# Kernel optimization log

Hardware: AMD Instinct MI355X
Metric: run time of the kernel (lower is better)

## Reference

```python
import jax, jax.numpy as jnp
import numpy as np

WS = 8       # window size
NH = 6       # num heads
SHIFT = 4    # ws//2 since index=1 (shifted)
EPS = 1e-6


def _rel_pos_index(ws):
    coords = np.stack(np.meshgrid(np.arange(ws), np.arange(ws), indexing='ij'))  # (2,ws,ws)
    cf = coords.reshape(2, -1)
    rel = (cf[:, :, None] - cf[:, None, :]).transpose(1, 2, 0)  # (N,N,2)
    rel[..., 0] += ws - 1
    rel[..., 1] += ws - 1
    rel[..., 0] *= 2 * ws - 1
    return rel.sum(-1)  # (N,N) int


def _attn_mask(H, W, ws, shift):
    img = np.zeros((H, W))
    slices = (slice(0, -ws), slice(-ws, -shift), slice(-shift, None))
    cnt = 0
    for h in slices:
        for w in slices:
            img[h, w] = cnt
            cnt += 1
    mw = img.reshape(H // ws, ws, W // ws, ws).transpose(0, 2, 1, 3).reshape(-1, ws * ws)
    am = mw[:, None, :] - mw[:, :, None]  # (nW,N,N): unsqueeze(1) - unsqueeze(2)
    return np.where(am != 0, -100.0, 0.0).astype(np.float32)


def layernorm2d(x, w, b):
    mu = x.mean(1, keepdims=True)
    var = ((x - mu) ** 2).mean(1, keepdims=True)
    y = (x - mu) / jnp.sqrt(var + EPS)
    return w[None, :, None, None] * y + b[None, :, None, None]


def window_partition(x, ws):
    B, C, H, W = x.shape
    x = x.reshape(B, C, H // ws, ws, W // ws, ws)
    return x.transpose(0, 2, 4, 3, 5, 1).reshape(-1, ws * ws, C)


def window_reverse(win, ws, H, W):
    B = win.shape[0] // ((H // ws) * (W // ws))
    x = win.reshape(B, H // ws, W // ws, ws, ws, -1)
    return x.transpose(0, 5, 1, 3, 2, 4).reshape(B, -1, H, W)


def shifted_window_attn(x, qkv_w, qkv_b, proj_w, proj_b, rpb_table):
    B, C, H, W = x.shape
    N = WS * WS
    hd = C // NH
    scale = hd ** -0.5
    # faithful to original: raw reshape BCHW->BHWC (reinterpretation), roll, reshape back
    x = jnp.roll(x.reshape(B, H, W, C), (-SHIFT, -SHIFT), (1, 2)).reshape(B, C, H, W)
    win = window_partition(x, WS)  # (B_, N, C)
    B_ = win.shape[0]
    qkv = (win @ qkv_w + qkv_b).reshape(B_, N, 3, NH, hd).transpose(2, 0, 3, 1, 4)
    q, k, v = qkv[0] * scale, qkv[1], qkv[2]
    attn = jnp.einsum('bhnd,bhmd->bhnm', q, k)  # (B_,NH,N,N)
    rpi = _rel_pos_index(WS)
    bias = rpb_table[rpi.reshape(-1)].reshape(N, N, NH).transpose(2, 0, 1)
    attn = attn + bias[None]
    mask = jnp.asarray(_attn_mask(H, W, WS, SHIFT))  # (nW,N,N)
    nW = mask.shape[0]
    attn = attn.reshape(B_ // nW, nW, NH, N, N) + mask[None, :, None]
    attn = jax.nn.softmax(attn.reshape(B_, NH, N, N), axis=-1)
    out = jnp.einsum('bhnm,bhmd->bhnd', attn, v).transpose(0, 2, 1, 3).reshape(B_, N, C)
    out = out @ proj_w + proj_b
    return window_reverse(out, WS, H, W)


def channel_attention(y, ca_w, ca_b):
    gap = y.mean((2, 3))  # (B,C)
    s = jnp.einsum('bc,oc->bo', gap, ca_w) + ca_b  # 1x1 conv on pooled feature
    return s[:, :, None, None]


def mlp(y, fc1_w, fc1_b, fc2_w, fc2_b):
    B, C, H, W = y.shape
    t = y.transpose(0, 2, 3, 1)  # (B,H,W,C)
    t = jax.nn.gelu(t @ fc1_w + fc1_b, approximate=False)
    t = t @ fc2_w + fc2_b
    return t.transpose(0, 3, 1, 2)


def setup_inputs() -> dict:
    key = jax.random.key(0)
    ks = jax.random.split(key, 8)
    C, H, W, B = 192, 256, 256, 2
    hid = 2 * C
    sc = 0.02
    return {
        'x': jax.random.normal(ks[0], (B, C, H, W), jnp.float32),
        'norm1_w': jnp.ones((C,), jnp.float32),
        'norm1_b': jnp.zeros((C,), jnp.float32),
        'qkv_w': jax.random.normal(ks[1], (C, 3 * C), jnp.float32) * sc,
        'qkv_b': jnp.zeros((3 * C,), jnp.float32),
        'proj_w': jax.random.normal(ks[2], (C, C), jnp.float32) * sc,
        'proj_b': jnp.zeros((C,), jnp.float32),
        'rpb_table': jax.random.normal(ks[3], ((2 * WS - 1) ** 2, NH), jnp.float32) * sc,
        'ca_w': jax.random.normal(ks[4], (C, C), jnp.float32) * sc,
        'ca_b': jnp.zeros((C,), jnp.float32),
        'norm2_w': jnp.ones((C,), jnp.float32),
        'norm2_b': jnp.zeros((C,), jnp.float32),
        'fc1_w': jax.random.normal(ks[5], (C, hid), jnp.float32) * sc,
        'fc1_b': jnp.zeros((hid,), jnp.float32),
        'fc2_w': jax.random.normal(ks[6], (hid, C), jnp.float32) * sc,
        'fc2_b': jnp.zeros((C,), jnp.float32),
    }


def reference(x, norm1_w, norm1_b, qkv_w, qkv_b, proj_w, proj_b, rpb_table,
              ca_w, ca_b, norm2_w, norm2_b, fc1_w, fc1_b, fc2_w, fc2_b):
    y = layernorm2d(x, norm1_w, norm1_b)
    y = shifted_window_attn(y, qkv_w, qkv_b, proj_w, proj_b, rpb_table)
    y = y * channel_attention(y, ca_w, ca_b)
    x = x + y
    y2 = mlp(layernorm2d(x, norm2_w, norm2_b), fc1_w, fc1_b, fc2_w, fc2_b)
    return x + y2
```

## Files before the change

kernel.cpp:

```cpp
#include <hip/hip_runtime.h>
#include <hip/hip_bf16.h>
#include <stdint.h>

#define C_   192
#define H_   256
#define W_   256
#define HW_  65536
#define CHW  12582912
#define NH_  6
#define HID_ 384

typedef __attribute__((ext_vector_type(8))) __bf16 bf16x8;
typedef __attribute__((ext_vector_type(8))) uint16_t u16x8;
typedef __attribute__((ext_vector_type(4))) float  fx4;

__device__ __forceinline__ uint16_t f2bf(float f) {
  uint32_t u = __builtin_bit_cast(uint32_t, f);
  u += 0x7fffu + ((u >> 16) & 1u);
  return (uint16_t)(u >> 16);
}
__device__ __forceinline__ float bf2f(uint16_t h) {
  uint32_t u = ((uint32_t)h) << 16;
  return __builtin_bit_cast(float, u);
}
__device__ __forceinline__ uint32_t pk2(float a, float b) {
  return (uint32_t)f2bf(a) | ((uint32_t)f2bf(b) << 16);
}
__device__ __forceinline__ bf16x8 ld8(const uint16_t* p) {
  uint4 v = *reinterpret_cast<const uint4*>(p);
  return __builtin_bit_cast(bf16x8, v);
}
__device__ __forceinline__ fx4 mfma16(bf16x8 a, bf16x8 b, fx4 c) {
  return __builtin_amdgcn_mfma_f32_16x16x32_bf16(a, b, c, 0, 0, 0);
}
__device__ __forceinline__ float gelu_f(float v) {
  float c2 = v * v;
  float u = __builtin_fmaf(c2, 0.044715f, 1.0f) * v;
  float e = exp2f(u * 2.3022084f);
  float th = 1.0f - 2.0f * __builtin_amdgcn_rcpf(1.0f + e);
  float hv = 0.5f * v;
  return __builtin_fmaf(hv, th, hv);
}

__global__ __launch_bounds__(256) void prep_kernel(
    const float* __restrict__ qkv_w, const float* __restrict__ proj_w,
    const float* __restrict__ fc1_w, const float* __restrict__ fc2_w,
    const float* __restrict__ rpb, const float* __restrict__ n2w,
    const float* __restrict__ n2b, const float* __restrict__ fc1_b,
    uint16_t* __restrict__ qkv_wt, uint16_t* __restrict__ proj_wt,
    uint16_t* __restrict__ fc1_wt, uint16_t* __restrict__ fc2_wt,
    float* __restrict__ rpbb, float* __restrict__ b1f) {
  int tid = blockIdx.x * 256 + threadIdx.x;
  if (tid < 576 * 192) {
    int f = tid / 192, k = tid % 192;
    qkv_wt[tid] = f2bf(qkv_w[k * 576 + f]);
  }
  int t1 = tid - 576 * 192;
  if (t1 >= 0 && t1 < 192 * 192) {
    int f = t1 / 192, k = t1 % 192;
    proj_wt[t1] = f2bf(proj_w[k * 192 + f]);
  }
  int t2 = t1 - 192 * 192;
  if (t2 >= 0 && t2 < 384 * 192) {
    int f = t2 / 192, k = t2 % 192;
    fc1_wt[t2] = f2bf(fc1_w[k * 384 + f] * n2w[k]);
  }
  int t3 = t2 - 384 * 192;
  if (t3 >= 0 && t3 < 192 * 384) {
    int f = t3 / 384, k = t3 % 384;
    fc2_wt[t3] = f2bf(fc2_w[k * 192 + f]);
  }
  int t4 = t3 - 192 * 384;
  if (t4 >= 0 && t4 < 6 * 64 * 64) {
    int h = t4 / 4096, nm = t4 % 4096, n = nm / 64, m = nm % 64;
    int yn = n >> 3, xn = n & 7, ym = m >> 3, xm = m & 7;
    int idx = (yn - ym + 7) * 15 + (xn - xm + 7);
    rpbb[t4] = rpb[idx * NH_ + h];
  }
  int t5 = t4 - 6 * 64 * 64;
  if (t5 >= 0 && t5 < 384) {
    float acc = fc1_b[t5];
    for (int c = 0; c < 192; c++) acc = __builtin_fmaf(n2b[c], fc1_w[c * 384 + t5], acc);
    b1f[t5] = acc;
  }
}

__global__ __launch_bounds__(256) void ln1_stats(const float* __restrict__ x,
                                                 float* __restrict__ mu,
                                                 float* __restrict__ rsig) {
  int t = blockIdx.x * 256 + threadIdx.x;
  int b = t >> 16, hw = t & 65535;
  const float* xp = x + (size_t)b * CHW + hw;
  float s = 0.f, sq = 0.f;
#pragma unroll 8
  for (int c = 0; c < C_; c++) {
    float v = xp[(size_t)c * HW_];
    s += v; sq += v * v;
  }
  float m = s * (1.0f / C_);
  float var = sq * (1.0f / C_) - m * m;
  mu[t] = m;
  rsig[t] = rsqrtf(var + 1e-6f);
}

__global__ __launch_bounds__(256) void ln1_apply_kernel(
    const float* __restrict__ x, const float* __restrict__ mu, const float* __restrict__ rsig,
    const float* __restrict__ n1w, const float* __restrict__ n1b,
    uint16_t* __restrict__ y_tok) {
  __shared__ __attribute__((aligned(16))) uint16_t tile[192 * 66];
  int wg = blockIdx.x;
  int b = wg >> 10, hw0 = (wg & 1023) << 6;
  int t = threadIdx.x;
  const float* xb = x + (size_t)b * CHW;
  const float* mub = mu + b * HW_;
  const float* rsb = rsig + b * HW_;
#pragma unroll 4
  for (int it = 0; it < 48; it++) {
    int id = it * 256 + t;
    int ca = id >> 6, pp = id & 63;
    int g = ca * 65536 + hw0 + pp;
    int h2 = g / 49152;
    int r = g - h2 * 49152;
    int w2 = r / 192;
    int c2 = r - w2 * 192;
    int f = ((h2 + 4) & 255) * 49152 + ((w2 + 4) & 255) * 192 + c2;
    int cnat = f >> 16;
    int hwn = f & 65535;
    float v = (xb[f] - mub[hwn]) * rsb[hwn] * n1w[cnat] + n1b[cnat];
    tile[ca * 66 + pp] = f2bf(v);
  }
  __syncthreads();
  uint16_t* yb = y_tok + ((size_t)(b * HW_ + hw0)) * C_;
#pragma unroll 4
  for (int it = 0; it < 48; it++) {
    int id = it * 256 + t;
    int pp = id / 192, ca = id - pp * 192;
    yb[id] = tile[ca * 66 + pp];
  }
}

__global__ __launch_bounds__(256, 2) void attn_kernel(
    const uint16_t* __restrict__ y_tok, const uint16_t* __restrict__ qkv_wt,
    const float* __restrict__ qkv_b, const uint16_t* __restrict__ proj_wt,
    const float* __restrict__ proj_b, const float* __restrict__ rpbb,
    uint16_t* __restrict__ y_attn, float* __restrict__ part) {
  __shared__ __attribute__((aligned(16))) uint16_t Qs[64 * 200];
  __shared__ __attribute__((aligned(16))) uint16_t Ks[64 * 200];
  __shared__ __attribute__((aligned(16))) uint16_t VT[32 * 72];
  __shared__ __attribute__((aligned(16))) uint16_t Ps[64 * 72];
  const int wg = blockIdx.x;
  const int b = wg >> 10, wid = wg & 1023;
  const int wh = wid >> 5, ww = wid & 31;
  const int t = threadIdx.x;
  const int w = t >> 6, l = t & 63;
  const int lane16 = l & 15, quad = l >> 4;
  const int trow = w * 16 + quad * 4;

  bf16x8 afr[4][6];
#pragma unroll
  for (int m = 0; m < 4; m++) {
    const int tok = m * 16 + lane16;
    const uint16_t* ap = y_tok +
        ((size_t)(b * HW_ + (wh * 8 + (tok >> 3)) * W_ + ww * 8 + (tok & 7))) * C_ + quad * 8;
#pragma unroll
    for (int k = 0; k < 6; k++) afr[m][k] = ld8(ap + k * 32);
  }

  const float scale = 0.17677669529663687f;
  uint32_t vpack[3][4][2];

#pragma unroll
  for (int j = 0; j < 3; j++) {
    const int nt = w + 4 * j;
    const uint16_t* bp = qkv_wt + (nt * 16 + lane16) * C_ + quad * 8;
    bf16x8 bfr[6];
#pragma unroll
    for (int k = 0; k < 6; k++) bfr[k] = ld8(bp + k * 32);
    fx4 acc[4];
#pragma unroll
    for (int m = 0; m < 4; m++) acc[m] = fx4{0.f, 0.f, 0.f, 0.f};
#pragma unroll
    for (int k = 0; k < 6; k++)
#pragma unroll
      for (int m = 0; m < 4; m++) acc[m] = mfma16(afr[m][k], bfr[k], acc[m]);
    const int f = nt * 16 + lane16;
    const float bias = qkv_b[f];
#pragma unroll
    for (int m = 0; m < 4; m++)
#pragma unroll
      for (int r = 0; r < 4; r++)
        Qs[(m * 16 + quad * 4 + r) * 200 + f] = f2bf((acc[m][r] + bias) * scale);
  }
#pragma unroll
  for (int j = 3; j < 6; j++) {
    const int nt = w + 4 * j;
    const uint16_t* bp = qkv_wt + (nt * 16 + lane16) * C_ + quad * 8;
    bf16x8 bfr[6];
#pragma unroll
    for (int k = 0; k < 6; k++) bfr[k] = ld8(bp + k * 32);
    fx4 acc[4];
#pragma unroll
    for (int m = 0; m < 4; m++) acc[m] = fx4{0.f, 0.f, 0.f, 0.f};
#pragma unroll
    for (int k = 0; k < 6; k++)
#pragma unroll
      for (int m = 0; m < 4; m++) acc[m] = mfma16(afr[m][k], bfr[k], acc[m]);
    const int f = nt * 16 + lane16;
    const float bias = qkv_b[f];
#pragma unroll
    for (int m = 0; m < 4; m++)
#pragma unroll
      for (int r = 0; r < 4; r++)
        Ks[(m * 16 + quad * 4 + r) * 200 + (f - 192)] = f2bf(acc[m][r] + bias);
  }
#pragma unroll
  for (int j = 6; j < 9; j++) {
    const int nt = w + 4 * j;
    const uint16_t* bp = qkv_wt + (nt * 16 + lane16) * C_ + quad * 8;
    bf16x8 bfr[6];
#pragma unroll
    for (int k = 0; k < 6; k++) bfr[k] = ld8(bp + k * 32);
    fx4 acc[4];
#pragma unroll
    for (int m = 0; m < 4; m++) acc[m] = fx4{0.f, 0.f, 0.f, 0.f};
#pragma unroll
    for (int k = 0; k < 6; k++)
#pragma unroll
      for (int m = 0; m < 4; m++) acc[m] = mfma16(afr[m][k], bfr[k], acc[m]);
    const float bias = qkv_b[nt * 16 + lane16];
    const int jv = j - 6;
#pragma unroll
    for (int m = 0; m < 4; m++) {
      vpack[jv][m][0] = pk2(acc[m][0] + bias, acc[m][1] + bias);
      vpack[jv][m][1] = pk2(acc[m][2] + bias, acc[m][3] + bias);
    }
  }

  const bool whe = (wh == 31), wwe = (ww == 31);

  for (int h = 0; h < 6; h++) {
    __syncthreads();
    {
      const int vt0 = 2 * h, vt1 = 2 * h + 1;
      if (w == (vt0 & 3)) {
        const int jv = vt0 >> 2;
#pragma unroll
        for (int m = 0; m < 4; m++) {
          uint2 vv; vv.x = vpack[jv][m][0]; vv.y = vpack[jv][m][1];
          *reinterpret_cast<uint2*>(&VT[lane16 * 72 + m * 16 + quad * 4]) = vv;
        }
      }
      if (w == (vt1 & 3)) {
        const int jv = vt1 >> 2;
#pragma unroll
        for (int m = 0; m < 4; m++) {
          uint2 vv; vv.x = vpack[jv][m][0]; vv.y = vpack[jv][m][1];
          *reinterpret_cast<uint2*>(&VT[(16 + lane16) * 72 + m * 16 + quad * 4]) = vv;
        }
      }
    }
    __syncthreads();

    const bf16x8 qa = ld8(&Qs[(w * 16 + lane16) * 200 + h * 32 + quad * 8]);
    fx4 sacc[4];
#pragma unroll
    for (int nt = 0; nt < 4; nt++) {
      const bf16x8 kb = ld8(&Ks[(nt * 16 + lane16) * 200 + h * 32 + quad * 8]);
      fx4 z = {0.f, 0.f, 0.f, 0.f};
      sacc[nt] = mfma16(qa, kb, z);
    }
    const float* rb = rpbb + h * 4096;
#pragma unroll
    for (int nt = 0; nt < 4; nt++) {
      const int ct = nt * 16 + lane16;
      const bool rbc = whe && ((ct >> 3) >= 4);
      const bool cbc = wwe && ((ct & 7) >= 4);
#pragma unroll
      for (int r = 0; r < 4; r++) {
        const int rt = trow + r;
        const bool rbr = whe && ((rt >> 3) >= 4);
        const bool cbr = wwe && ((rt & 7) >= 4);
        float v = sacc[nt][r] + rb[rt * 64 + ct];
        if (rbr != rbc || cbr != cbc) v -= 100.f;
        sacc[nt][r] = v;
      }
    }
    float sm[4];
#pragma unroll
    for (int r = 0; r < 4; r++) {
      float m = fmaxf(fmaxf(sacc[0][r], sacc[1][r]), fmaxf(sacc[2][r], sacc[3][r]));
      m = fmaxf(m, __shfl_xor(m, 1));
      m = fmaxf(m, __shfl_xor(m, 2));
      m = fmaxf(m, __shfl_xor(m, 4));
      m = fmaxf(m, __shfl_xor(m, 8));
      float s0 = 0.f;
#pragma unroll
      for (int nt = 0; nt < 4; nt++) {
        float e = exp2f((sacc[nt][r] - m) * 1.4426950408889634f);
        sacc[nt][r] = e; s0 += e;
      }
      s0 += __shfl_xor(s0, 1);
      s0 += __shfl_xor(s0, 2);
      s0 += __shfl_xor(s0, 4);
      s0 += __shfl_xor(s0, 8);
      sm[r] = s0;
    }
#pragma unroll
    for (int nt = 0; nt < 4; nt++)
#pragma unroll
      for (int r = 0; r < 4; r++)
        Ps[(trow + r) * 72 + nt * 16 + lane16] = f2bf(sacc[nt][r]);
    fx4 o0 = {0.f, 0.f, 0.f, 0.f}, o1 = {0.f, 0.f, 0.f, 0.f};
#pragma unroll
    for (int ks2 = 0; ks2 < 2; ks2++) {
      const bf16x8 pa = ld8(&Ps[(w * 16 + lane16) * 72 + ks2 * 32 + quad * 8]);
      const bf16x8 v0 = ld8(&VT[(lane16) * 72 + ks2 * 32 + quad * 8]);
      const bf16x8 v1 = ld8(&VT[(16 + lane16) * 72 + ks2 * 32 + quad * 8]);
      o0 = mfma16(pa, v0, o0);
      o1 = mfma16(pa, v1, o1);
    }
#pragma unroll
    for (int r = 0; r < 4; r++) {
      const float inv = 1.0f / sm[r];
      Qs[(trow + r) * 200 + h * 32 + lane16] = f2bf(o0[r] * inv);
      Qs[(trow + r) * 200 + h * 32 + 16 + lane16] = f2bf(o1[r] * inv);
    }
  }
  __syncthreads();

  bf16x8 ofr[4][6];
#pragma unroll
  for (int m = 0; m < 4; m++)
#pragma unroll
    for (int k = 0; k < 6; k++)
      ofr[m][k] = ld8(&Qs[(m * 16 + lane16) * 200 + k * 32 + quad * 8]);

  uint16_t* yb = y_attn + (size_t)b * HW_ * C_;
  uint32_t obase[4][4];
#pragma unroll
  for (int m = 0; m < 4; m++)
#pragma unroll
    for (int r = 0; r < 4; r++) {
      const int tok = m * 16 + quad * 4 + r;
      obase[m][r] = (uint32_t)(((wh * 8 + (tok >> 3)) * W_ + ww * 8 + (tok & 7)) * C_);
    }
#pragma unroll
  for (int j = 0; j < 3; j++) {
    const int nt = w + 4 * j;
    const uint16_t* bp = proj_wt + (nt * 16 + lane16) * C_ + quad * 8;
    bf16x8 bfr[6];
#pragma unroll
    for (int k = 0; k < 6; k++) bfr[k] = ld8(bp + k * 32);
    fx4 acc[4];
#pragma unroll
    for (int m = 0; m < 4; m++) acc[m] = fx4{0.f, 0.f, 0.f, 0.f};
#pragma unroll
    for (int k = 0; k < 6; k++)
#pragma unroll
      for (int m = 0; m < 4; m++) acc[m] = mfma16(ofr[m][k], bfr[k], acc[m]);
    const float pb = proj_b[nt * 16 + lane16];
    float cs = 0.f;
#pragma unroll
    for (int m = 0; m < 4; m++)
#pragma unroll
      for (int r = 0; r < 4; r++) {
        const float v = acc[m][r] + pb;
        yb[obase[m][r] + nt * 16 + lane16] = f2bf(v);
        cs += v;
      }
    cs += __shfl_xor(cs, 16);
    cs += __shfl_xor(cs, 32);
    if (l < 16) part[(size_t)wg * 192 + nt * 16 + lane16] = cs;
  }
}

__global__ __launch_bounds__(768) void ca_s_kernel(const float* __restrict__ part,
                                                   const float* __restrict__ ca_w,
                                                   const float* __restrict__ ca_b,
                                                   float* __restrict__ sbuf) {
  int b = blockIdx.x;
  int t = threadIdx.x;
  __shared__ float red[768];
  __shared__ float gap[192];
  int g = t / 192, c = t - g * 192;
  float s = 0.f;
#pragma unroll 8
  for (int i = g; i < 1024; i += 4) s += part[((size_t)b * 1024 + i) * 192 + c];
  red[t] = s;
  __syncthreads();
  if (t < 192)
    gap[t] = (red[t] + red[t + 192] + red[t + 384] + red[t + 576]) * (1.0f / 65536.0f);
  __syncthreads();
  if (t < 192) {
    float acc = ca_b[t];
#pragma unroll 8
    for (int c2 = 0; c2 < 192; c2++) acc += gap[c2] * ca_w[t * 192 + c2];
    sbuf[b * 192 + t] = acc;
  }
}

__global__ __launch_bounds__(512, 4) void fused_mlp(
    const float* __restrict__ x, const uint16_t* __restrict__ y_attn,
    const float* __restrict__ sbuf,
    const uint16_t* __restrict__ fc1_wt, const float* __restrict__ b1f,
    const uint16_t* __restrict__ fc2_wt, const float* __restrict__ fc2_b,
    float* __restrict__ out) {
  __shared__ __attribute__((aligned(16))) char smem[192 * 66 * 4];
  __shared__ float red[512];
  __shared__ float mus[128];
  __shared__ float sarr[192];
  float* tileXR = (float*)smem;
  uint16_t* hbuf = (uint16_t*)smem;
  float* ftile = (float*)smem;
  const int wg = blockIdx.x;
  const int b = wg >> 10, hw0 = (wg & 1023) << 6;
  const int t = threadIdx.x;
  const int w = t >> 6, l = t & 63;
  const int lane16 = l & 15, quad = l >> 4;

  if (t < 192) sarr[t] = sbuf[b * 192 + t];

  const float* xb = x + (size_t)b * CHW + hw0;
#pragma unroll
  for (int i = 0; i < 12; i++) {
    int id = i * 512 + t;
    int c = id >> 5, p2 = id & 31;
    float2 v = *reinterpret_cast<const float2*>(xb + (size_t)c * HW_ + p2 * 2);
    *reinterpret_cast<float2*>(&tileXR[c * 66 + p2 * 2]) = v;
  }
  __syncthreads();

  {
    const int p = t & 63, qb = (t >> 6) * 3;
    const uint16_t* yr = y_attn + ((size_t)(b * HW_ + hw0 + p)) * C_;
#pragma unroll
    for (int i = 0; i < 3; i++) {
      int q = qb + i;
      u16x8 uv = __builtin_bit_cast(u16x8, ld8(yr + q * 8));
#pragma unroll
      for (int j = 0; j < 8; j++) {
        int c = q * 8 + j;
        tileXR[c * 66 + p] += sarr[c] * bf2f(uv[j]);
      }
    }
  }
  __syncthreads();

  if (t < 256) {
    int p = t & 63, g = t >> 6;
    float s = 0.f, sq = 0.f;
#pragma unroll 8
    for (int c = g * 48; c < g * 48 + 48; c++) {
      float v = tileXR[c * 66 + p];
      s += v; sq += v * v;
    }
    red[g * 64 + p] = s;
    red[256 + g * 64 + p] = sq;
  }
  __syncthreads();
  if (t < 64) {
    float ss = red[t] + red[64 + t] + red[128 + t] + red[192 + t];
    float qq = red[256 + t] + red[320 + t] + red[384 + t] + red[448 + t];
    float m = ss * (1.0f / C_);
    float var = qq * (1.0f / C_) - m * m;
    mus[t] = m;
    mus[64 + t] = rsqrtf(var + 1e-6f);
  }
  __syncthreads();

  bf16x8 afr[6];
  const int m1 = w & 3;
  {
    const int p = m1 * 16 + lane16;
    const float mu = mus[p], rs = mus[64 + p];
#pragma unroll
    for (int k = 0; k < 6; k++) {
      uint32_t u0, u1, u2, u3;
      {
        int c = k * 32 + quad * 8;
        float a0 = (tileXR[(c + 0) * 66 + p] - mu) * rs;
        float a1 = (tileXR[(c + 1) * 66 + p] - mu) * rs;
        float a2 = (tileXR[(c + 2) * 66 + p] - mu) * rs;
        float a3 = (tileXR[(c + 3) * 66 + p] - mu) * rs;
        float a4 = (tileXR[(c + 4) * 66 + p] - mu) * rs;
        float a5 = (tileXR[(c + 5) * 66 + p] - mu) * rs;
        float a6 = (tileXR[(c + 6) * 66 + p] - mu) * rs;
        float a7 = (tileXR[(c + 7) * 66 + p] - mu) * rs;
        u0 = pk2(a0, a1); u1 = pk2(a2, a3); u2 = pk2(a4, a5); u3 = pk2(a6, a7);
      }
      uint4 uv = {u0, u1, u2, u3};
      afr[k] = __builtin_bit_cast(bf16x8, uv);
    }
  }
  __syncthreads();

  {
    const int ntb = (w >> 2) * 12;
#pragma unroll 4
    for (int j = 0; j < 12; j++) {
      const int nt = ntb + j;
      const uint16_t* bp = fc1_wt + (nt * 16 + lane16) * C_ + quad * 8;
      bf16x8 bfr[6];
#pragma unroll
      for (int k = 0; k < 6; k++) bfr[k] = ld8(bp + k * 32);
      fx4 acc = {0.f, 0.f, 0.f, 0.f};
#pragma unroll
      for (int k = 0; k < 6; k++) acc = mfma16(bfr[k], afr[k], acc);
      const fx4 b4 = *reinterpret_cast<const fx4*>(b1f + nt * 16 + quad * 4);
      float g0 = gelu_f(acc[0] + b4[0]);
      float g1 = gelu_f(acc[1] + b4[1]);
      float g2 = gelu_f(acc[2] + b4[2]);
      float g3 = gelu_f(acc[3] + b4[3]);
      uint2 wv = {pk2(g0, g1), pk2(g2, g3)};
      *reinterpret_cast<uint2*>(&hbuf[(m1 * 16 + lane16) * 392 + nt * 16 + quad * 4]) = wv;
    }
  }
  __syncthreads();

  const int mh2 = w >> 2;
  const int ntr2 = w & 3;
  fx4 acc2[3][2];
#pragma unroll
  for (int j = 0; j < 3; j++)
#pragma unroll
    for (int mi = 0; mi < 2; mi++) acc2[j][mi] = fx4{0.f, 0.f, 0.f, 0.f};
#pragma unroll
  for (int kc = 0; kc < 4; kc++) {
#pragma unroll
    for (int kk = 0; kk < 3; kk++) {
      bf16x8 ha0 = ld8(&hbuf[((mh2 * 2 + 0) * 16 + lane16) * 392 + kc * 96 + kk * 32 + quad * 8]);
      bf16x8 ha1 = ld8(&hbuf[((mh2 * 2 + 1) * 16 + lane16) * 392 + kc * 96 + kk * 32 + quad * 8]);
#pragma unroll
      for (int j = 0; j < 3; j++) {
        const int nt2 = ntr2 * 3 + j;
        const bf16x8 bb = ld8(fc2_wt + (nt2 * 16 + lane16) * HID_ + kc * 96 + kk * 32 + quad * 8);
        acc2[j][0] = mfma16(ha0, bb, acc2[j][0]);
        acc2[j][1] = mfma16(ha1, bb, acc2[j][1]);
      }
    }
  }
  __syncthreads();

#pragma unroll
  for (int j = 0; j < 3; j++) {
    const int nt2 = ntr2 * 3 + j;
    const float bias = fc2_b[nt2 * 16 + lane16];
#pragma unroll
    for (int mi = 0; mi < 2; mi++) {
      float* fp = &ftile[(nt2 * 16 + lane16) * 66 + (mh2 * 2 + mi) * 16 + quad * 4];
      float2 aa = {acc2[j][mi][0] + bias, acc2[j][mi][1] + bias};
      float2 bb2 = {acc2[j][mi][2] + bias, acc2[j][mi][3] + bias};
      *reinterpret_cast<float2*>(fp) = aa;
      *reinterpret_cast<float2*>(fp + 2) = bb2;
    }
  }
  __syncthreads();

  {
    const int p = t & 63, qb = (t >> 6) * 3;
    const uint16_t* yr = y_attn + ((size_t)(b * HW_ + hw0 + p)) * C_;
#pragma unroll
    for (int i = 0; i < 3; i++) {
      int q = qb + i;
      u16x8 uv = __builtin_bit_cast(u16x8, ld8(yr + q * 8));
#pragma unroll
      for (int j = 0; j < 8; j++) {
        int c = q * 8 + j;
        ftile[c * 66 + p] += sarr[c] * bf2f(uv[j]);
      }
    }
  }
  __syncthreads();

  float* ob = out + (size_t)b * CHW + hw0;
#pragma unroll
  for (int i = 0; i < 12; i++) {
    int id = i * 512 + t;
    int c = id >> 5, p2 = id & 31;
    float2 xv = *reinterpret_cast<const float2*>(xb + (size_t)c * HW_ + p2 * 2);
    float2 fv = *reinterpret_cast<const float2*>(&ftile[c * 66 + p2 * 2]);
    float2 ov = {xv.x + fv.x, xv.y + fv.y};
    *reinterpret_cast<float2*>(ob + (size_t)c * HW_ + p2 * 2) = ov;
  }
}

extern "C" void kernel_launch(void* const* d_in, const int* in_sizes, int n_in,
                              void* d_out, int out_size, void* d_ws, size_t ws_size,
                              hipStream_t stream) {
  const float* x      = (const float*)d_in[0];
  const float* n1w    = (const float*)d_in[1];
  const float* n1b    = (const float*)d_in[2];
  const float* qkv_w  = (const float*)d_in[3];
  const float* qkv_b  = (const float*)d_in[4];
  const float* proj_w = (const float*)d_in[5];
  const float* proj_b = (const float*)d_in[6];
  const float* rpb    = (const float*)d_in[7];
  const float* ca_w   = (const float*)d_in[8];
  const float* ca_b   = (const float*)d_in[9];
  const float* n2w    = (const float*)d_in[10];
  const float* n2b    = (const float*)d_in[11];
  const float* fc1_w  = (const float*)d_in[12];
  const float* fc1_b  = (const float*)d_in[13];
  const float* fc2_w  = (const float*)d_in[14];
  const float* fc2_b  = (const float*)d_in[15];
  float* out = (float*)d_out;

  char* ws = (char*)d_ws;
  uint16_t* y_tok   = (uint16_t*)(ws + 0);
  uint16_t* y_attn  = (uint16_t*)(ws + 50331648);
  float*    mu      = (float*)   (ws + 100663296);
  float*    rsig    = (float*)   (ws + 101187584);
  uint16_t* qkv_wt  = (uint16_t*)(ws + 101711872);
  uint16_t* proj_wt = (uint16_t*)(ws + 101933056);
  uint16_t* fc1_wt  = (uint16_t*)(ws + 102006784);
  uint16_t* fc2_wt  = (uint16_t*)(ws + 102154240);
  float*    rpbb    = (float*)   (ws + 102301696);
  float*    part    = (float*)   (ws + 102400000);
  float*    sbuf    = (float*)   (ws + 103972864);
  float*    b1f     = (float*)   (ws + 103974400);

  hipLaunchKernelGGL(prep_kernel, dim3(1250), dim3(256), 0, stream,
                     qkv_w, proj_w, fc1_w, fc2_w, rpb, n2w, n2b, fc1_b,
                     qkv_wt, proj_wt, fc1_wt, fc2_wt, rpbb, b1f);
  hipLaunchKernelGGL(ln1_stats, dim3(512), dim3(256), 0, stream, x, mu, rsig);
  hipLaunchKernelGGL(ln1_apply_kernel, dim3(2048), dim3(256), 0, stream,
                     x, mu, rsig, n1w, n1b, y_tok);
  hipLaunchKernelGGL(attn_kernel, dim3(2048), dim3(256), 0, stream,
                     y_tok, qkv_wt, qkv_b, proj_wt, proj_b, rpbb, y_attn, part);
  hipLaunchKernelGGL(ca_s_kernel, dim3(2), dim3(768), 0, stream, part, ca_w, ca_b, sbuf);
  hipLaunchKernelGGL(fused_mlp, dim3(2048), dim3(512), 0, stream,
                     x, y_attn, sbuf, fc1_wt, b1f, fc2_wt, fc2_b, out);
}
```

Measured before the change: 617.8 us.

## Fuse residual-add and LayerNorm stats into registers, store bf16 tile in LDS

The fused MLP kernel no longer stages the fp32 x tile in shared memory. Each thread now loads x directly from global memory, adds the scaled attention output, and accumulates per-pixel sum and sum-of-squares in registers. It writes a bf16 pixel-major tile to LDS, and the normalization statistics are reduced from 8 partial sums inside the MFMA fragment build. The final residual is also computed straight from global x and y_attn into the output without a separate tile pass. This cuts LDS traffic and footprint and removes several barriers. In exchange, the residual is stored in bf16 before LayerNorm, which loses precision, and x is now read with per-thread strided scalar loads.

```diff
diff --git a/kernel.cpp b/kernel.cpp
--- a/kernel.cpp
+++ b/kernel.cpp
@@ -406,10 +406,8 @@
     const uint16_t* __restrict__ fc2_wt, const float* __restrict__ fc2_b,
     float* __restrict__ out) {
   __shared__ __attribute__((aligned(16))) char smem[192 * 66 * 4];
-  __shared__ float red[512];
-  __shared__ float mus[128];
-  __shared__ float sarr[192];
-  float* tileXR = (float*)smem;
+  uint16_t* tileX = (uint16_t*)smem;
+  float* red = (float*)(smem + 25600);
   uint16_t* hbuf = (uint16_t*)smem;
   float* ftile = (float*)smem;
   const int wg = blockIdx.x;
@@ -417,78 +415,58 @@
   const int t = threadIdx.x;
   const int w = t >> 6, l = t & 63;
   const int lane16 = l & 15, quad = l >> 4;
-
-  if (t < 192) sarr[t] = sbuf[b * 192 + t];
-
-  const float* xb = x + (size_t)b * CHW + hw0;
-#pragma unroll
-  for (int i = 0; i < 12; i++) {
-    int id = i * 512 + t;
-    int c = id >> 5, p2 = id & 31;
-    float2 v = *reinterpret_cast<const float2*>(xb + (size_t)c * HW_ + p2 * 2);
-    *reinterpret_cast<float2*>(&tileXR[c * 66 + p2 * 2]) = v;
-  }
-  __syncthreads();
+  const int p = l;
+  const int q = w;
+  const int c0 = q * 24;
+
+  const float* xb = x + (size_t)b * CHW + hw0 + p;
+  const uint16_t* yr = y_attn + ((size_t)(b * HW_ + hw0 + p)) * C_ + c0;
+  const float* sb = sbuf + b * 192 + c0;
 
   {
-    const int p = t & 63, qb = (t >> 6) * 3;
-    const uint16_t* yr = y_attn + ((size_t)(b * HW_ + hw0 + p)) * C_;
-#pragma unroll
-    for (int i = 0; i < 3; i++) {
-      int q = qb + i;
-      u16x8 uv = __builtin_bit_cast(u16x8, ld8(yr + q * 8));
+    float ssum = 0.f, sqsum = 0.f;
+#pragma unroll
+    for (int g = 0; g < 3; g++) {
+      u16x8 yv = __builtin_bit_cast(u16x8, ld8(yr + g * 8));
+      fx4 s0 = *reinterpret_cast<const fx4*>(sb + g * 8);
+      fx4 s1 = *reinterpret_cast<const fx4*>(sb + g * 8 + 4);
+      float xr[8];
 #pragma unroll
       for (int j = 0; j < 8; j++) {
-        int c = q * 8 + j;
-        tileXR[c * 66 + p] += sarr[c] * bf2f(uv[j]);
-      }
-    }
-  }
-  __syncthreads();
-
-  if (t < 256) {
-    int p = t & 63, g = t >> 6;
-    float s = 0.f, sq = 0.f;
-#pragma unroll 8
-    for (int c = g * 48; c < g * 48 + 48; c++) {
-      float v = tileXR[c * 66 + p];
-      s += v; sq += v * v;
-    }
-    red[g * 64 + p] = s;
-    red[256 + g * 64 + p] = sq;
-  }
-  __syncthreads();
-  if (t < 64) {
-    float ss = red[t] + red[64 + t] + red[128 + t] + red[192 + t];
-    float qq = red[256 + t] + red[320 + t] + red[384 + t] + red[448 + t];
-    float m = ss * (1.0f / C_);
-    float var = qq * (1.0f / C_) - m * m;
-    mus[t] = m;
-    mus[64 + t] = rsqrtf(var + 1e-6f);
+        float sv = (j < 4) ? s0[j] : s1[j - 4];
+        float v = __builtin_fmaf(sv, bf2f(yv[j]), xb[(size_t)(c0 + g * 8 + j) * HW_]);
+        xr[j] = v;
+        ssum += v; sqsum = __builtin_fmaf(v, v, sqsum);
+      }
+      uint4 w4 = {pk2(xr[0], xr[1]), pk2(xr[2], xr[3]),
+                  pk2(xr[4], xr[5]), pk2(xr[6], xr[7])};
+      *reinterpret_cast<uint4*>(&tileX[p * 200 + c0 + g * 8]) = w4;
+    }
+    red[q * 64 + p] = ssum;
+    red[512 + q * 64 + p] = sqsum;
   }
   __syncthreads();
 
   bf16x8 afr[6];
   const int m1 = w & 3;
   {
-    const int p = m1 * 16 + lane16;
-    const float mu = mus[p], rs = mus[64 + p];
+    const int p3 = m1 * 16 + lane16;
+    float ss = 0.f, qq = 0.f;
+#pragma unroll
+    for (int qi = 0; qi < 8; qi++) {
+      ss += red[qi * 64 + p3];
+      qq += red[512 + qi * 64 + p3];
+    }
+    const float mu = ss * (1.0f / C_);
+    const float rs = rsqrtf(qq * (1.0f / C_) - mu * mu + 1e-6f);
 #pragma unroll
     for (int k = 0; k < 6; k++) {
-      uint32_t u0, u1, u2, u3;
-      {
-        int c = k * 32 + quad * 8;
-        float a0 = (tileXR[(c + 0) * 66 + p] - mu) * rs;
-        float a1 = (tileXR[(c + 1) * 66 + p] - mu) * rs;
-        float a2 = (tileXR[(c + 2) * 66 + p] - mu) * rs;
-        float a3 = (tileXR[(c + 3) * 66 + p] - mu) * rs;
-        float a4 = (tileXR[(c + 4) * 66 + p] - mu) * rs;
-        float a5 = (tileXR[(c + 5) * 66 + p] - mu) * rs;
-        float a6 = (tileXR[(c + 6) * 66 + p] - mu) * rs;
-        float a7 = (tileXR[(c + 7) * 66 + p] - mu) * rs;
-        u0 = pk2(a0, a1); u1 = pk2(a2, a3); u2 = pk2(a4, a5); u3 = pk2(a6, a7);
-      }
-      uint4 uv = {u0, u1, u2, u3};
+      u16x8 xv = __builtin_bit_cast(u16x8, ld8(&tileX[p3 * 200 + k * 32 + quad * 8]));
+      float a0 = (bf2f(xv[0]) - mu) * rs, a1 = (bf2f(xv[1]) - mu) * rs;
+      float a2 = (bf2f(xv[2]) - mu) * rs, a3 = (bf2f(xv[3]) - mu) * rs;
+      float a4 = (bf2f(xv[4]) - mu) * rs, a5 = (bf2f(xv[5]) - mu) * rs;
+      float a6 = (bf2f(xv[6]) - mu) * rs, a7 = (bf2f(xv[7]) - mu) * rs;
+      uint4 uv = {pk2(a0, a1), pk2(a2, a3), pk2(a4, a5), pk2(a6, a7)};
       afr[k] = __builtin_bit_cast(bf16x8, uv);
     }
   }
@@ -556,31 +534,19 @@
   }
   __syncthreads();
 
-  {
-    const int p = t & 63, qb = (t >> 6) * 3;
-    const uint16_t* yr = y_attn + ((size_t)(b * HW_ + hw0 + p)) * C_;
-#pragma unroll
-    for (int i = 0; i < 3; i++) {
-      int q = qb + i;
-      u16x8 uv = __builtin_bit_cast(u16x8, ld8(yr + q * 8));
-#pragma unroll
-      for (int j = 0; j < 8; j++) {
-        int c = q * 8 + j;
-        ftile[c * 66 + p] += sarr[c] * bf2f(uv[j]);
-      }
-    }
-  }
-  __syncthreads();
-
-  float* ob = out + (size_t)b * CHW + hw0;
-#pragma unroll
-  for (int i = 0; i < 12; i++) {
-    int id = i * 512 + t;
-    int c = id >> 5, p2 = id & 31;
-    float2 xv = *reinterpret_cast<const float2*>(xb + (size_t)c * HW_ + p2 * 2);
-    float2 fv = *reinterpret_cast<const float2*>(&ftile[c * 66 + p2 * 2]);
-    float2 ov = {xv.x + fv.x, xv.y + fv.y};
-    *reinterpret_cast<float2*>(ob + (size_t)c * HW_ + p2 * 2) = ov;
+  float* ob = out + (size_t)b * CHW + hw0 + p;
+#pragma unroll
+  for (int g = 0; g < 3; g++) {
+    u16x8 yv = __builtin_bit_cast(u16x8, ld8(yr + g * 8));
+    fx4 s0 = *reinterpret_cast<const fx4*>(sb + g * 8);
+    fx4 s1 = *reinterpret_cast<const fx4*>(sb + g * 8 + 4);
+#pragma unroll
+    for (int j = 0; j < 8; j++) {
+      const int c = c0 + g * 8 + j;
+      float sv = (j < 4) ? s0[j] : s1[j - 4];
+      float v = ftile[c * 66 + p] + xb[(size_t)c * HW_] + sv * bf2f(yv[j]);
+      ob[(size_t)c * HW_] = v;
+    }
   }
 }
 
```

Result: slower. 715.9 us (+15.9%).
